# Performance work log

Hardware: AMD Instinct MI355X
Metric: run time of the kernel (lower is better)

## Reference

```python
import jax, jax.numpy as jnp
import numpy as np

ANCHORS = np.array([[10,13],[16,30],[33,23],[30,61],[62,45],[59,119],[116,90],[156,198],[373,326]], dtype=np.float32)
MASKS = [[6,7,8],[3,4,5],[0,1,2]]
IMG = 416
STRIDES = [8,16,32]  # img//52, img//26, img//13
NUM_CLASSES = 20
L_COORD, L_OBJ, L_NOOBJ, L_CLS = 5.0, 1.0, 0.5, 1.0


def _bce(p, t):
    # F.binary_cross_entropy with mean reduction; clip keeps log finite (torch clamps at -100)
    eps = 1e-12
    return -jnp.mean(t * jnp.log(jnp.clip(p, eps, 1.0)) + (1.0 - t) * jnp.log(jnp.clip(1.0 - p, eps, 1.0)))


def _mse(a, b):
    return jnp.mean((a - b) ** 2)


def _scale_loss(pred, boxes, cls_idx, anchors_s, fs):
    B = pred.shape[0]
    A = anchors_s.shape[0]  # 3
    C = NUM_CLASSES
    pred = pred.reshape(B, fs, fs, A, 5 + C)
    coords = jnp.arange(fs, dtype=pred.dtype)
    # decode: (B, fs, fs, A)
    pred_cx = jax.nn.sigmoid(pred[..., 0]) + coords[None, None, :, None]  # x varies along dim 2
    pred_cy = jax.nn.sigmoid(pred[..., 1]) + coords[None, :, None, None]
    aw, ah = anchors_s[:, 0], anchors_s[:, 1]
    pred_w = jnp.exp(pred[..., 2]) * aw
    pred_h = jnp.exp(pred[..., 3]) * ah
    pred_conf = jax.nn.sigmoid(pred[..., 4])
    pred_cls = jax.nn.sigmoid(pred[..., 5:])  # (B, fs, fs, A, C)

    # --- target assignment (vectorized over B and T) ---
    tb = boxes * fs                      # (B, T, 4) in grid units
    tw, th = tb[..., 2], tb[..., 3]
    # IoU of [0,0,w,h] boxes centered at origin -> min-overlap
    inter = jnp.minimum(tw[..., None], aw) * jnp.minimum(th[..., None], ah)  # (B,T,A)
    union = (tw * th)[..., None] + aw * ah - inter
    best = jnp.argmax(inter / (union + 1e-6), axis=-1)  # (B, T)
    gx = jnp.clip(tb[..., 0].astype(jnp.int32), 0, fs - 1)
    gy = jnp.clip(tb[..., 1].astype(jnp.int32), 0, fs - 1)
    bidx = jnp.broadcast_to(jnp.arange(B, dtype=jnp.int32)[:, None], best.shape)
    flat = (((bidx * fs + gy) * fs + gx) * A + best.astype(jnp.int32)).ravel()  # (B*T,)
    N = B * fs * fs * A

    def scat(v):
        return jnp.zeros((N,), pred.dtype).at[flat].set(v.ravel()).reshape(B, fs, fs, A)

    obj = scat(jnp.ones_like(tw))
    noobj = 1.0 - obj
    tcx = scat(tb[..., 0] - gx.astype(pred.dtype))
    tcy = scat(tb[..., 1] - gy.astype(pred.dtype))
    tww = scat(jnp.log(tw / aw[best] + 1e-6))
    thh = scat(jnp.log(th / ah[best] + 1e-6))
    tconf = obj
    tcls = jnp.zeros((N, C), pred.dtype).at[flat, cls_idx.ravel()].set(1.0).reshape(B, fs, fs, A, C)

    loss_coord = (_mse(pred_cx * obj, tcx * obj) + _mse(pred_cy * obj, tcy * obj)
                  + _mse(pred_w * obj, tww * obj) + _mse(pred_h * obj, thh * obj)) * L_COORD
    loss_conf = _bce(pred_conf * obj, tconf * obj) * L_OBJ + _bce(pred_conf * noobj, tconf * noobj) * L_NOOBJ
    m = obj[..., None]
    loss_cls = _bce(pred_cls * m, tcls * m) * L_CLS
    return loss_coord + loss_conf + loss_cls


def reference(pred0, pred1, pred2, target_boxes, target_cls):
    total = 0.0
    for i, (pred, s) in enumerate(zip([pred0, pred1, pred2], STRIDES)):
        fs = IMG // s
        anchors_s = jnp.asarray(ANCHORS[MASKS[i]]) / s
        total = total + _scale_loss(pred, target_boxes, target_cls, anchors_s, fs)
    return total / 3.0


def setup_inputs() -> dict:
    key = jax.random.key(0)
    k0, k1, k2, kb, kc = jax.random.split(key, 5)
    B, T = 64, 50
    return {
        "pred0": jax.random.normal(k0, (B, 52, 52, 75), dtype=jnp.float32),
        "pred1": jax.random.normal(k1, (B, 26, 26, 75), dtype=jnp.float32),
        "pred2": jax.random.normal(k2, (B, 13, 13, 75), dtype=jnp.float32),
        "target_boxes": jax.random.uniform(kb, (B, T, 4), dtype=jnp.float32),
        "target_cls": jax.random.randint(kc, (B, T), 0, 20, dtype=jnp.int32),
    }
```

## Files before the change

### kernel.cpp

```cpp
#include <hip/hip_runtime.h>
#include <math.h>

#define NT 50
#define NC 20
#define NB 64
#define NCORR 192
#define NS0 1585
#define NS1 397
#define NS2 100
#define NSTREAM (NS0 + NS1 + NS2)
#define NBLK (NCORR + NSTREAM)
#define CHUNK 2048

__device__ __constant__ float c_aw[3][3] = {
    {14.5f, 19.5f, 46.625f},
    {1.875f, 3.875f, 3.6875f},
    {0.3125f, 0.5f, 1.03125f}};
__device__ __constant__ float c_ah[3][3] = {
    {11.25f, 24.75f, 40.75f},
    {3.8125f, 2.8125f, 7.4375f},
    {0.40625f, 0.9375f, 0.71875f}};
__device__ __constant__ float c_invN[3] = {
    1.0f / 519168.0f, 1.0f / 129792.0f, 1.0f / 32448.0f};

__device__ __forceinline__ float softplus_f(float x) {
  return __logf(1.0f + __expf(x));
}
__device__ __forceinline__ float sigmoid_f(float x) {
  return 1.0f / (1.0f + __expf(-x));
}

__global__ __launch_bounds__(256) void yolo_main(
    const float* __restrict__ pred0, const float* __restrict__ pred1,
    const float* __restrict__ pred2, const float* __restrict__ boxes,
    const int* __restrict__ cls, float* __restrict__ ws) {
  const int bid = blockIdx.x;
  const int tid = threadIdx.x;
  __shared__ float s_red[4];
  float acc = 0.0f;

  if (bid >= NCORR) {
    int sb = bid - NCORR;
    int scale, part, nf4;
    const float* arr;
    if (sb < NS0) { scale = 0; part = sb; arr = pred0; nf4 = 3244800; }
    else if (sb < NS0 + NS1) { scale = 1; part = sb - NS0; arr = pred1; nf4 = 811200; }
    else { scale = 2; part = sb - NS0 - NS1; arr = pred2; nf4 = 202800; }
    const float4* p4 = (const float4*)arr;
    const int base = part * CHUNK;
    const int i0 = base + tid;
    int ch = ((i0 << 2) % 25);
    if (base + CHUNK <= nf4) {
#pragma unroll
      for (int k = 0; k < 8; ++k) {
        float4 v = p4[i0 + 256 * k];
        float vc = (ch == 4) ? v.x : ((ch == 3) ? v.y : ((ch == 2) ? v.z : v.w));
        bool take = (ch >= 1) && (ch <= 4);
        acc += take ? softplus_f(vc) : 0.0f;
        ch = (ch >= 1) ? (ch - 1) : 24;
      }
    } else {
      for (int i = i0; i < nf4; i += 256) {
        float4 v = p4[i];
        float vc = (ch == 4) ? v.x : ((ch == 3) ? v.y : ((ch == 2) ? v.z : v.w));
        bool take = (ch >= 1) && (ch <= 4);
        acc += take ? softplus_f(vc) : 0.0f;
        ch = (ch >= 1) ? (ch - 1) : 24;
      }
    }
    acc *= c_invN[scale] * (0.5f / 3.0f);
  } else {
    const int scale = bid >> 6;
    const int b = bid & 63;
    const int fs = (scale == 0) ? 52 : ((scale == 1) ? 26 : 13);
    const int cells = fs * fs * 3;
    const float* arr = (scale == 0) ? pred0 : ((scale == 1) ? pred1 : pred2);
    const float* plane = arr + (size_t)b * cells * 25;
    const float invN = c_invN[scale];
    const float invNC = invN * (1.0f / (float)NC);

    __shared__ int s_cell[NT];
    __shared__ unsigned s_bit[NT];

    int cell = -1, gx = 0, gy = 0, best = 0;
    float tcx = 0.f, tcy = 0.f, tww = 0.f, thh = 0.f;
    if (tid < NT) {
      const float* bx = boxes + ((size_t)b * NT + tid) * 4;
      float ffs = (float)fs;
      float tbx = bx[0] * ffs;
      float tby = bx[1] * ffs;
      float tw = bx[2] * ffs;
      float th = bx[3] * ffs;
      float bestr = -1.0f;
      for (int a = 0; a < 3; ++a) {
        float aw = c_aw[scale][a], ah = c_ah[scale][a];
        float inter = fminf(tw, aw) * fminf(th, ah);
        float uni = tw * th + aw * ah - inter;
        float rr = inter / (uni + 1e-6f);
        if (rr > bestr) { bestr = rr; best = a; }
      }
      gx = (int)tbx;
      if (gx < 0) gx = 0;
      if (gx > fs - 1) gx = fs - 1;
      gy = (int)tby;
      if (gy < 0) gy = 0;
      if (gy > fs - 1) gy = fs - 1;
      cell = (gy * fs + gx) * 3 + best;
      tcx = tbx - (float)gx;
      tcy = tby - (float)gy;
      tww = __logf(tw / c_aw[scale][best] + 1e-6f);
      thh = __logf(th / c_ah[scale][best] + 1e-6f);
      s_cell[tid] = cell;
      s_bit[tid] = 1u << cls[(size_t)b * NT + tid];
    }
    __syncthreads();
    if (tid < NT) {
      int win = -1;
      unsigned mask = 0u;
      for (int t = 0; t < NT; ++t)
        if (s_cell[t] == cell) { win = t; mask |= s_bit[t]; }
      if (win == tid) {
        const float* p = plane + cell * 25;
        float aw = c_aw[scale][best], ah = c_ah[scale][best];
        float d0 = sigmoid_f(p[0]) + (float)gx - tcx;
        float d1 = sigmoid_f(p[1]) + (float)gy - tcy;
        float d2 = __expf(p[2]) * aw - tww;
        float d3 = __expf(p[3]) * ah - thh;
        float coord = 5.0f * invN * (d0 * d0 + d1 * d1 + d2 * d2 + d3 * d3);
        float v4 = p[4];
        float conf = invN * softplus_f(-v4) - 0.5f * invN * softplus_f(v4);
        float csum = 0.0f;
        for (int c = 0; c < NC; ++c) {
          float v = p[5 + c];
          csum += ((mask >> c) & 1u) ? softplus_f(-v) : softplus_f(v);
        }
        acc = (coord + conf + csum * invNC) * (1.0f / 3.0f);
      }
    }
  }

  for (int off = 32; off > 0; off >>= 1) acc += __shfl_down(acc, off);
  if ((tid & 63) == 0) s_red[tid >> 6] = acc;
  __syncthreads();
  if (tid == 0) ws[bid] = s_red[0] + s_red[1] + s_red[2] + s_red[3];
}

__global__ __launch_bounds__(1024) void reduce_kernel(
    const float* __restrict__ ws, float* __restrict__ out) {
  __shared__ float s_red[16];
  int tid = threadIdx.x;
  float v = 0.0f;
  for (int i = tid; i < NBLK; i += 1024) v += ws[i];
  for (int off = 32; off > 0; off >>= 1) v += __shfl_down(v, off);
  if ((tid & 63) == 0) s_red[tid >> 6] = v;
  __syncthreads();
  if (tid == 0) {
    float s = 0.0f;
#pragma unroll
    for (int i = 0; i < 16; ++i) s += s_red[i];
    out[0] = s;
  }
}

extern "C" void kernel_launch(void* const* d_in, const int* in_sizes, int n_in,
                              void* d_out, int out_size, void* d_ws, size_t ws_size,
                              hipStream_t stream) {
  const float* pred0 = (const float*)d_in[0];
  const float* pred1 = (const float*)d_in[1];
  const float* pred2 = (const float*)d_in[2];
  const float* boxes = (const float*)d_in[3];
  const int* cls = (const int*)d_in[4];
  float* out = (float*)d_out;
  float* ws = (float*)d_ws;

  yolo_main<<<NBLK, 256, 0, stream>>>(pred0, pred1, pred2, boxes, cls, ws);
  reduce_kernel<<<1, 1024, 0, stream>>>(ws, out);
}
```

Measured before the change: 20.74 us.

## Fuse final reduction via atomic last-block counters and enlarge streaming chunks

The separate single-block reduce kernel is removed. Each block now writes its partial sum and bumps one of 32 padded atomic counters, plus a second-level counter, so the last finishing block sums all partials and writes the output. Each streaming block also handles four times more float4 data, which cuts the grid from 2274 to 714 blocks. The trade-off is a hipMemsetAsync to zero the counters before every launch, plus atomic and fence overhead, and less parallelism per scale.

```diff
diff --git a/kernel.cpp b/kernel.cpp
--- a/kernel.cpp
+++ b/kernel.cpp
@@ -5,12 +5,13 @@
 #define NC 20
 #define NB 64
 #define NCORR 192
-#define NS0 1585
-#define NS1 397
-#define NS2 100
+#define CH4 8192
+#define NS0 397
+#define NS1 100
+#define NS2 25
 #define NSTREAM (NS0 + NS1 + NS2)
 #define NBLK (NCORR + NSTREAM)
-#define CHUNK 2048
+#define CNT_OFF 4096
 
 __device__ __constant__ float c_aw[3][3] = {
     {14.5f, 19.5f, 46.625f},
@@ -33,10 +34,12 @@
 __global__ __launch_bounds__(256) void yolo_main(
     const float* __restrict__ pred0, const float* __restrict__ pred1,
     const float* __restrict__ pred2, const float* __restrict__ boxes,
-    const int* __restrict__ cls, float* __restrict__ ws) {
+    const int* __restrict__ cls, float* __restrict__ ws, int* __restrict__ cnt,
+    float* __restrict__ out) {
   const int bid = blockIdx.x;
   const int tid = threadIdx.x;
   __shared__ float s_red[4];
+  __shared__ int s_fin;
   float acc = 0.0f;
 
   if (bid >= NCORR) {
@@ -47,24 +50,24 @@
     else if (sb < NS0 + NS1) { scale = 1; part = sb - NS0; arr = pred1; nf4 = 811200; }
     else { scale = 2; part = sb - NS0 - NS1; arr = pred2; nf4 = 202800; }
     const float4* p4 = (const float4*)arr;
-    const int base = part * CHUNK;
+    const int base = part * CH4;
     const int i0 = base + tid;
-    int ch = ((i0 << 2) % 25);
-    if (base + CHUNK <= nf4) {
+    int ch = (i0 << 2) % 25;
+    if (base + CH4 <= nf4) {
+      for (int o = 0; o < 4; ++o) {
 #pragma unroll
-      for (int k = 0; k < 8; ++k) {
-        float4 v = p4[i0 + 256 * k];
-        float vc = (ch == 4) ? v.x : ((ch == 3) ? v.y : ((ch == 2) ? v.z : v.w));
-        bool take = (ch >= 1) && (ch <= 4);
-        acc += take ? softplus_f(vc) : 0.0f;
-        ch = (ch >= 1) ? (ch - 1) : 24;
+        for (int k = 0; k < 8; ++k) {
+          float4 v = p4[i0 + o * 2048 + k * 256];
+          float vc = (ch == 4) ? v.x : ((ch == 3) ? v.y : ((ch == 2) ? v.z : v.w));
+          acc += (ch >= 1 && ch <= 4) ? softplus_f(vc) : 0.0f;
+          ch = (ch >= 1) ? (ch - 1) : 24;
+        }
       }
     } else {
       for (int i = i0; i < nf4; i += 256) {
         float4 v = p4[i];
         float vc = (ch == 4) ? v.x : ((ch == 3) ? v.y : ((ch == 2) ? v.z : v.w));
-        bool take = (ch >= 1) && (ch <= 4);
-        acc += take ? softplus_f(vc) : 0.0f;
+        acc += (ch >= 1 && ch <= 4) ? softplus_f(vc) : 0.0f;
         ch = (ch >= 1) ? (ch - 1) : 24;
       }
     }
@@ -142,23 +145,35 @@
   for (int off = 32; off > 0; off >>= 1) acc += __shfl_down(acc, off);
   if ((tid & 63) == 0) s_red[tid >> 6] = acc;
   __syncthreads();
-  if (tid == 0) ws[bid] = s_red[0] + s_red[1] + s_red[2] + s_red[3];
-}
 
-__global__ __launch_bounds__(1024) void reduce_kernel(
-    const float* __restrict__ ws, float* __restrict__ out) {
-  __shared__ float s_red[16];
-  int tid = threadIdx.x;
-  float v = 0.0f;
-  for (int i = tid; i < NBLK; i += 1024) v += ws[i];
-  for (int off = 32; off > 0; off >>= 1) v += __shfl_down(v, off);
-  if ((tid & 63) == 0) s_red[tid >> 6] = v;
+  if (tid == 0) {
+    ws[bid] = s_red[0] + s_red[1] + s_red[2] + s_red[3];
+    __threadfence();
+    const int line = bid & 31;
+    const int quota = 22 + (line < (NBLK & 31) ? 1 : 0);
+    int fin = 0;
+    int old = atomicAdd(&cnt[line * 16], 1);
+    if (old == quota - 1) {
+      int old2 = atomicAdd(&cnt[32 * 16], 1);
+      if (old2 == 31) fin = 1;
+    }
+    s_fin = fin;
+  }
   __syncthreads();
-  if (tid == 0) {
-    float s = 0.0f;
+
+  if (s_fin) {
+    __threadfence();
+    float v = 0.0f;
 #pragma unroll
-    for (int i = 0; i < 16; ++i) s += s_red[i];
-    out[0] = s;
+    for (int k = 0; k < 3; ++k) {
+      int i = tid + k * 256;
+      if (i < NBLK)
+        v += __hip_atomic_load(&ws[i], __ATOMIC_RELAXED, __HIP_MEMORY_SCOPE_AGENT);
+    }
+    for (int off = 32; off > 0; off >>= 1) v += __shfl_down(v, off);
+    if ((tid & 63) == 0) s_red[tid >> 6] = v;
+    __syncthreads();
+    if (tid == 0) out[0] = s_red[0] + s_red[1] + s_red[2] + s_red[3];
   }
 }
 
@@ -172,7 +187,8 @@
   const int* cls = (const int*)d_in[4];
   float* out = (float*)d_out;
   float* ws = (float*)d_ws;
+  int* cnt = (int*)((char*)d_ws + CNT_OFF);
 
-  yolo_main<<<NBLK, 256, 0, stream>>>(pred0, pred1, pred2, boxes, cls, ws);
-  reduce_kernel<<<1, 1024, 0, stream>>>(ws, out);
+  hipMemsetAsync((void*)cnt, 0, 33 * 64, stream);
+  yolo_main<<<NBLK, 256, 0, stream>>>(pred0, pred1, pred2, boxes, cls, ws, cnt, out);
 }
```

Result: slower. 45.73 us (+120.5%).
